# Kernel tuning notes

Hardware: AMD Instinct MI355X
Metric: run time of the kernel (lower is better)

The kernel has to match this reference:

```python
import jax, jax.numpy as jnp
import numpy as np

B, T, D_IN, D_OUT, H = 128, 128, 64, 64, 1024


def _lstm_cell(x_t, h, c, W_ih, W_hh, b_ih, b_hh):
    # PyTorch LSTMCell: gates = x@W_ih^T + b_ih + h@W_hh^T + b_hh, order [i, f, g, o]
    g = x_t @ W_ih.T + b_ih + h @ W_hh.T + b_hh  # [B, 4H]
    i, f, gg, o = jnp.split(g, 4, axis=-1)
    c_new = jax.nn.sigmoid(f) * c + jax.nn.sigmoid(i) * jnp.tanh(gg)
    h_new = jax.nn.sigmoid(o) * jnp.tanh(c_new)
    return h_new, c_new


def setup_inputs() -> dict:
    key = jax.random.key(0)
    ks = jax.random.split(key, 16)
    s_in = 1.0 / np.sqrt(H)
    inp = {
        "x": jax.random.normal(ks[0], (B, T, D_IN), dtype=jnp.float32),
        "W_ih1": jax.random.normal(ks[1], (4 * H, D_IN), dtype=jnp.float32) * s_in,
        "W_hh1": jax.random.normal(ks[2], (4 * H, H), dtype=jnp.float32) * s_in,
        "b_ih1": jax.random.normal(ks[3], (4 * H,), dtype=jnp.float32) * s_in,
        "b_hh1": jax.random.normal(ks[4], (4 * H,), dtype=jnp.float32) * s_in,
        "W_ih2": jax.random.normal(ks[5], (4 * H, H), dtype=jnp.float32) * s_in,
        "W_hh2": jax.random.normal(ks[6], (4 * H, H), dtype=jnp.float32) * s_in,
        "b_ih2": jax.random.normal(ks[7], (4 * H,), dtype=jnp.float32) * s_in,
        "b_hh2": jax.random.normal(ks[8], (4 * H,), dtype=jnp.float32) * s_in,
        "W_lin": jax.random.normal(ks[9], (D_IN, H), dtype=jnp.float32) * s_in,
        "b_lin": jax.random.normal(ks[10], (D_IN,), dtype=jnp.float32) * s_in,
        "W_hio": jax.random.normal(ks[11], (D_OUT, H), dtype=jnp.float32) * s_in,
        "b_hio": jax.random.normal(ks[12], (D_OUT,), dtype=jnp.float32) * s_in,
        "future": 1,
    }
    return inp


def reference(x, W_ih1, W_hh1, b_ih1, b_hh1, W_ih2, W_hh2, b_ih2, b_hh2,
              W_lin, b_lin, W_hio, b_hio, future):
    b = x.shape[0]
    h1 = jnp.zeros((b, H), x.dtype)
    c1 = jnp.zeros((b, H), x.dtype)
    h2 = jnp.zeros((b, H), x.dtype)
    c2 = jnp.zeros((b, H), x.dtype)

    def step(carry, x_t):
        h1, c1, h2, c2 = carry
        h1, c1 = _lstm_cell(x_t, h1, c1, W_ih1, W_hh1, b_ih1, b_hh1)
        h2, c2 = _lstm_cell(h1, h2, c2, W_ih2, W_hh2, b_ih2, b_hh2)
        return (h1, c1, h2, c2), None

    (h1, c1, h2, c2), _ = jax.lax.scan(step, (h1, c1, h2, c2),
                                       jnp.swapaxes(x, 0, 1))  # scan over T
    output = h2 @ W_lin.T + b_lin  # [B, D_IN] (only last step's value is used)

    for _ in range(int(future)):
        h1, c1 = _lstm_cell(output, h1, c1, W_ih1, W_hh1, b_ih1, b_hh1)
        h2, c2 = _lstm_cell(h1, h2, c2, W_ih2, W_hh2, b_ih2, b_hh2)
        output = h2 @ W_hio.T + b_hio  # [B, D_OUT]

    return output[:, None, :]  # [B, 1, D_OUT]
```

## Files before the change

kernel.cpp:

```cpp
#include <hip/hip_runtime.h>

#define B_   128
#define T_   128
#define DIN  64
#define H_   1024
#define NBLK 256
#define NTHR 1024

typedef _Float16 f16;
typedef _Float16 half8 __attribute__((ext_vector_type(8)));
typedef float float4v __attribute__((ext_vector_type(4)));
typedef unsigned uint2v __attribute__((ext_vector_type(2)));
typedef unsigned uint4v __attribute__((ext_vector_type(4)));

#define OFF_W2    34816
#define OFF_SG1A  100352
#define OFF_SG1B  109056
#define OFF_SG2A  117760
#define OFF_SG2B  126464
#define OFF_C1    135168
#define OFF_C2    137216
#define OFF_B1    139264
#define OFF_B2    139328
#define SMEM_BYTES 139392

struct Params {
  const float *x, *Wih1, *Whh1, *bih1, *bhh1, *Wih2, *Whh2, *bih2, *bhh2,
              *Wlin, *blin, *Whio, *bhio;
  const int* fut;
  float* out;
  f16 *x16, *h1a, *h1b, *h2a, *h2b, *ob;
  unsigned *arrive, *rel;
  unsigned *S;
  float* PB;
  unsigned* FL;
};

__device__ __forceinline__ float sigm(float v) { return 1.f / (1.f + __expf(-v)); }
__device__ __forceinline__ float tanh_(float v) { return 2.f / (1.f + __expf(-2.f * v)) - 1.f; }

__device__ __forceinline__ unsigned get_xcc() {
  unsigned x;
  asm volatile("s_getreg_b32 %0, hwreg(HW_REG_XCC_ID)" : "=s"(x));
  return x & 15u;
}

__device__ __forceinline__ void grid_sync(unsigned* arrive, unsigned* rel, unsigned ph) {
  __syncthreads();
  const int tid = threadIdx.x, bid = blockIdx.x;
  if (bid == 0) {
    if (tid > 0 && tid < NBLK) {
      while (__hip_atomic_load(&arrive[tid], __ATOMIC_RELAXED, __HIP_MEMORY_SCOPE_AGENT) != ph)
        __builtin_amdgcn_s_sleep(8);
    }
    __syncthreads();
    if (tid == 0)
      __hip_atomic_store(rel, ph, __ATOMIC_RELEASE, __HIP_MEMORY_SCOPE_AGENT);
  } else {
    if (tid == 0) {
      __hip_atomic_store(&arrive[bid], ph, __ATOMIC_RELEASE, __HIP_MEMORY_SCOPE_AGENT);
      while (__hip_atomic_load(rel, __ATOMIC_RELAXED, __HIP_MEMORY_SCOPE_AGENT) != ph)
        __builtin_amdgcn_s_sleep(8);
    }
  }
  __syncthreads();
  __builtin_amdgcn_fence(__ATOMIC_ACQUIRE, "agent");
}

__device__ __forceinline__ void fast_sync(unsigned* S, unsigned x, unsigned xtotal,
                                          unsigned nxcd, unsigned ph) {
  __syncthreads();
  if (threadIdx.x == 0) {
    unsigned t = __hip_atomic_fetch_add(&S[x * 32], 1u, __ATOMIC_RELAXED, __HIP_MEMORY_SCOPE_AGENT);
    bool leader = (t % xtotal == 0u);
    if ((t + 1u) % xtotal == 0u) {
      unsigned c = __hip_atomic_fetch_add(&S[512], 1u, __ATOMIC_RELAXED, __HIP_MEMORY_SCOPE_AGENT);
      if ((c + 1u) % nxcd == 0u)
        __hip_atomic_store(&S[544], ph, __ATOMIC_RELAXED, __HIP_MEMORY_SCOPE_AGENT);
      asm volatile("buffer_inv sc0 sc1\n\ts_waitcnt vmcnt(0)" ::: "memory");
      __hip_atomic_store(&S[1088 + x * 32], ph, __ATOMIC_RELAXED, __HIP_MEMORY_SCOPE_AGENT);
    }
    if (leader) {
      while (__hip_atomic_load(&S[544], __ATOMIC_RELAXED, __HIP_MEMORY_SCOPE_AGENT) != ph)
        __builtin_amdgcn_s_sleep(1);
      while (__hip_atomic_load(&S[1088 + x * 32], __ATOMIC_RELAXED, __HIP_MEMORY_SCOPE_AGENT) != ph)
        __builtin_amdgcn_s_sleep(1);
      __hip_atomic_store(&S[576 + x * 32], ph, __ATOMIC_RELAXED, __HIP_MEMORY_SCOPE_AGENT);
      asm volatile("buffer_inv sc0\n\ts_waitcnt vmcnt(0)" ::: "memory");
    } else {
      while (__hip_atomic_load(&S[576 + x * 32], __ATOMIC_RELAXED, __HIP_MEMORY_SCOPE_AGENT) != ph)
        __builtin_amdgcn_s_sleep(2);
      asm volatile("buffer_inv sc0\n\ts_waitcnt vmcnt(0)" ::: "memory");
    }
  }
  __syncthreads();
}

__global__ void __launch_bounds__(NTHR, 4) lstm_k(Params p) {
  extern __shared__ char smem[];
  f16*   W1s  = (f16*)(smem);
  f16*   W2s  = (f16*)(smem + OFF_W2);
  float* Sg1A = (float*)(smem + OFF_SG1A);
  float* Sg1B = (float*)(smem + OFF_SG1B);
  float* Sg2A = (float*)(smem + OFF_SG2A);
  float* Sg2B = (float*)(smem + OFF_SG2B);
  float* c1   = (float*)(smem + OFF_C1);
  float* c2   = (float*)(smem + OFF_C2);
  float* bs1  = (float*)(smem + OFF_B1);
  float* bs2  = (float*)(smem + OFF_B2);

  const int tid = threadIdx.x, bid = blockIdx.x;
  const int c   = bid & 127;
  const int g   = bid >> 7;
  const int bidp = bid ^ 128;
  const int cb  = c * 2 + g;
  const int fut = p.fut[0];
  const unsigned xcc = get_xcc();
  unsigned* S = p.S;

  if (bid == 0) {
    for (int i = tid; i < 2048; i += NTHR)
      __hip_atomic_store(&S[i], 0u, __ATOMIC_RELAXED, __HIP_MEMORY_SCOPE_AGENT);
  }
  for (int i = bid * NTHR + tid; i < 256 * 32; i += NBLK * NTHR)
    __hip_atomic_store(&p.FL[i], 0u, __ATOMIC_RELAXED, __HIP_MEMORY_SCOPE_AGENT);

  for (int idx = tid; idx < 17 * 2 * 512; idx += NTHR) {
    int j2 = idx >> 9, r = idx & 511;
    int j = j2 >> 1, nt = j2 & 1;
    int lane_ = r >> 3, jj = r & 7;
    int q = lane_ >> 4, colw = lane_ & 15;
    int row = (colw >> 2) * H_ + c * 8 + nt * 4 + (colw & 3);
    float v = (j < 16) ? p.Whh1[row * H_ + g * 512 + j * 32 + q * 8 + jj]
                       : p.Wih1[row * DIN + g * 32 + q * 8 + jj];
    W1s[idx] = (f16)v;
  }
  for (int idx = tid; idx < 32 * 2 * 512; idx += NTHR) {
    int j2 = idx >> 9, r = idx & 511;
    int j = j2 >> 1, nt = j2 & 1;
    int lane_ = r >> 3, jj = r & 7;
    int q = lane_ >> 4, colw = lane_ & 15;
    int row = (colw >> 2) * H_ + c * 8 + nt * 4 + (colw & 3);
    float v = (j < 16) ? p.Wih2[row * H_ + g * 512 + j * 32 + q * 8 + jj]
                       : p.Whh2[row * H_ + g * 512 + (j - 16) * 32 + q * 8 + jj];
    W2s[idx] = (f16)v;
  }
  if (tid < 16) {
    int row = (tid >> 2) * H_ + c * 8 + g * 4 + (tid & 3);
    bs1[tid] = p.bih1[row] + p.bhh1[row];
    bs2[tid] = p.bih2[row] + p.bhh2[row];
  }
  for (int i = tid; i < 512; i += NTHR) { c1[i] = 0.f; c2[i] = 0.f; }
  for (int i = bid * NTHR + tid; i < B_ * T_ * DIN; i += NBLK * NTHR)
    p.x16[i] = (f16)p.x[i];
  for (int i = bid * NTHR + tid; i < B_ * H_; i += NBLK * NTHR) {
    p.h1a[i] = (f16)0.f; p.h1b[i] = (f16)0.f;
    p.h2a[i] = (f16)0.f; p.h2b[i] = (f16)0.f;
  }

  unsigned ph = 1;
  grid_sync(p.arrive, p.rel, ph);
  if (tid == 0)
    __hip_atomic_fetch_add(&S[1600 + xcc], 1u, __ATOMIC_RELAXED, __HIP_MEMORY_SCOPE_AGENT);
  ++ph;
  grid_sync(p.arrive, p.rel, ph);

  unsigned xtotal = __hip_atomic_load(&S[1600 + xcc], __ATOMIC_RELAXED, __HIP_MEMORY_SCOPE_AGENT);
  unsigned nxcd = 0;
  for (int i = 0; i < 16; ++i)
    nxcd += (__hip_atomic_load(&S[1600 + i], __ATOMIC_RELAXED, __HIP_MEMORY_SCOPE_AGENT) != 0u);

  auto gsync = [&]() { ++ph; fast_sync(S, xcc, xtotal, nxcd, ph); };

  const int lane = tid & 63, wq = tid >> 6;
  const int s  = wq >> 3;
  const int wv = wq & 7;
  const int col = lane & 15, quad = lane >> 4;
  const int m0 = wv * 16 + col;
  const int ko = quad * 8;
  const f16* W1f = W1s + lane * 8;
  const f16* W2f = W2s + lane * 8;
  float* S1w = s ? Sg1B : Sg1A;
  float* S2w = s ? Sg2B : Sg2A;
  const int hoff = quad * 1024 + m0 * 4;

  auto PBidx = [](int cg, int dg, int ss, int ll) {
    return ((((cg * 2 + dg) * 2 + ss) * 2 + ll) * 2048);
  };

  f16 *h1c = p.h1a, *h1n = p.h1b, *h2c = p.h2a, *h2n = p.h2b;
  unsigned pcnt = 0;

  auto lstm_pw = [&](const float* SgA, const float* SgB, float* Pb0, float* Pb1,
                     const float* bsX, float* cst, f16* hn) {
    int idx = tid & 511;
    int mm = idx >> 2, cc = idx & 3;
    int i0 = mm * 17 + cc;
    int pb = mm * 16 + cc;
    float gq[4];
    #pragma unroll
    for (int q = 0; q < 4; ++q) {
      float pv0 = __hip_atomic_load(Pb0 + pb + q * 4, __ATOMIC_RELAXED, __HIP_MEMORY_SCOPE_AGENT);
      float pv1 = __hip_atomic_load(Pb1 + pb + q * 4, __ATOMIC_RELAXED, __HIP_MEMORY_SCOPE_AGENT);
      gq[q] = SgA[i0 + q * 4] + SgB[i0 + q * 4] + pv0 + pv1 + bsX[q * 4 + cc];
    }
    float cn = sigm(gq[1]) * cst[idx] + sigm(gq[0]) * tanh_(gq[2]);
    cst[idx] = cn;
    f16 hv = (f16)(sigm(gq[3]) * tanh_(cn));
    int v = (int)__builtin_bit_cast(unsigned short, hv);
    int base = lane & ~3;
    int v0 = __shfl(v, base, 64),     v1 = __shfl(v, base + 1, 64);
    int v2 = __shfl(v, base + 2, 64), v3 = __shfl(v, base + 3, 64);
    if (cc == 0) {
      unsigned long long pk = (unsigned long long)(unsigned short)v0
        | ((unsigned long long)(unsigned short)v1 << 16)
        | ((unsigned long long)(unsigned short)v2 << 32)
        | ((unsigned long long)(unsigned short)v3 << 48);
      __hip_atomic_store((unsigned long long*)(hn + cb * 512 + mm * 4), pk,
                         __ATOMIC_RELAXED, __HIP_MEMORY_SCOPE_AGENT);
    }
  };

  auto ldwin = [&](const f16* hX, int j) -> half8 {
    const uint2v* q0 = (const uint2v*)(hX + j * 4096 + hoff);
    const uint2v* q1 = (const uint2v*)(hX + j * 4096 + hoff + 512);
    uint2v u0 = *q0, u1 = *q1;
    uint4v u = {u0[0], u0[1], u1[0], u1[1]};
    return __builtin_bit_cast(half8, u);
  };

  auto phase = [&](bool l1, bool l2, const f16* xp, int xstr) {
    ++pcnt;
    float4v a1A = {0,0,0,0}, a1B = {0,0,0,0};
    float4v a2A = {0,0,0,0}, a2B = {0,0,0,0};

    if (l1 && s == 0) {
      half8 ax = *(const half8*)(xp + m0 * xstr + g * 32 + ko);
      a1A = __builtin_amdgcn_mfma_f32_16x16x32_f16(ax, *(const half8*)(W1f + 32 * 512), a1A, 0, 0, 0);
      a1B = __builtin_amdgcn_mfma_f32_16x16x32_f16(ax, *(const half8*)(W1f + 33 * 512), a1B, 0, 0, 0);
    }
    #pragma unroll
    for (int i = 0; i < 8; ++i) {
      int j = s * 8 + i;
      int gw = g * 16 + j;
      half8 w1 = ldwin(h1c, gw);
      if (l1) {
        a1A = __builtin_amdgcn_mfma_f32_16x16x32_f16(w1, *(const half8*)(W1f + (j * 2) * 512), a1A, 0, 0, 0);
        a1B = __builtin_amdgcn_mfma_f32_16x16x32_f16(w1, *(const half8*)(W1f + (j * 2 + 1) * 512), a1B, 0, 0, 0);
      }
      if (l2) {
        half8 w2 = ldwin(h2c, gw);
        a2A = __builtin_amdgcn_mfma_f32_16x16x32_f16(w1, *(const half8*)(W2f + (j * 2) * 512), a2A, 0, 0, 0);
        a2B = __builtin_amdgcn_mfma_f32_16x16x32_f16(w1, *(const half8*)(W2f + (j * 2 + 1) * 512), a2B, 0, 0, 0);
        a2A = __builtin_amdgcn_mfma_f32_16x16x32_f16(w2, *(const half8*)(W2f + ((16 + j) * 2) * 512), a2A, 0, 0, 0);
        a2B = __builtin_amdgcn_mfma_f32_16x16x32_f16(w2, *(const half8*)(W2f + ((16 + j) * 2 + 1) * 512), a2B, 0, 0, 0);
      }
    }

    {
      int mb = (wv * 16 + quad * 4) * 16 + col;
      if (l1) {
        float4v pa = g ? a1A : a1B;
        float* dst = p.PB + PBidx(c, 1 - g, s, 0) + mb;
        #pragma unroll
        for (int r = 0; r < 4; ++r)
          __hip_atomic_store(dst + r * 16, pa[r], __ATOMIC_RELAXED, __HIP_MEMORY_SCOPE_AGENT);
      }
      if (l2) {
        float4v pa = g ? a2A : a2B;
        float* dst = p.PB + PBidx(c, 1 - g, s, 1) + mb;
        #pragma unroll
        for (int r = 0; r < 4; ++r)
          __hip_atomic_store(dst + r * 16, pa[r], __ATOMIC_RELAXED, __HIP_MEMORY_SCOPE_AGENT);
      }
    }
    __syncthreads();
    if (tid == 0)
      __hip_atomic_store(&p.FL[bid * 32], pcnt, __ATOMIC_RELEASE, __HIP_MEMORY_SCOPE_AGENT);

    if (l1) {
      float4v oa = g ? a1B : a1A;
      #pragma unroll
      for (int r = 0; r < 4; ++r)
        S1w[(wv * 16 + quad * 4 + r) * 17 + col] = oa[r];
    }
    if (l2) {
      float4v oa = g ? a2B : a2A;
      #pragma unroll
      for (int r = 0; r < 4; ++r)
        S2w[(wv * 16 + quad * 4 + r) * 17 + col] = oa[r];
    }
    __syncthreads();

    while (__hip_atomic_load(&p.FL[bidp * 32], __ATOMIC_RELAXED, __HIP_MEMORY_SCOPE_AGENT) < pcnt)
      __builtin_amdgcn_s_sleep(1);

    if (tid < 512) {
      if (l1) lstm_pw(Sg1A, Sg1B,
                      p.PB + PBidx(c, g, 0, 0), p.PB + PBidx(c, g, 1, 0),
                      bs1, c1, h1n);
    } else {
      if (l2) lstm_pw(Sg2A, Sg2B,
                      p.PB + PBidx(c, g, 0, 1), p.PB + PBidx(c, g, 1, 1),
                      bs2, c2, h2n);
    }
  };

  auto out_phase = [&](const float* W, const float* bv, bool wout) {
    if (tid >= 512) return;
    int j = bid & 63, mgp = bid >> 6;
    int rid = tid >> 4, ks = tid & 15;
    int mrow = mgp * 32 + rid;
    const float* wr = W + j * H_ + ks * 64;
    float sacc = 0.f;
    #pragma unroll
    for (int q = 0; q < 16; ++q) {
      const uint2v* hp = (const uint2v*)(h2c + (ks * 16 + q) * 512 + mrow * 4);
      uint2v u = *hp;
      half8 hv4;
      { uint4v t = {u[0], u[1], 0u, 0u}; hv4 = __builtin_bit_cast(half8, t); }
      sacc += (float)hv4[0] * wr[q * 4 + 0] + (float)hv4[1] * wr[q * 4 + 1]
            + (float)hv4[2] * wr[q * 4 + 2] + (float)hv4[3] * wr[q * 4 + 3];
    }
    sacc += __shfl_down(sacc, 8, 16);
    sacc += __shfl_down(sacc, 4, 16);
    sacc += __shfl_down(sacc, 2, 16);
    sacc += __shfl_down(sacc, 1, 16);
    if (ks == 0) {
      float v = sacc + bv[j];
      f16 hv = (f16)v;
      __hip_atomic_store((unsigned short*)&p.ob[mrow * 64 + j],
                         __builtin_bit_cast(unsigned short, hv),
                         __ATOMIC_RELAXED, __HIP_MEMORY_SCOPE_AGENT);
      if (wout) p.out[mrow * 64 + j] = v;
    }
  };

  for (int t = -1; t < T_; ++t) {
    bool l1 = (t + 1 < T_), l2 = (t >= 0);
    phase(l1, l2, p.x16 + (t + 1) * DIN, T_ * DIN);
    gsync();
    if (l1) { f16* tm = h1c; h1c = h1n; h1n = tm; }
    if (l2) { f16* tm = h2c; h2c = h2n; h2n = tm; }
  }
  out_phase(p.Wlin, p.blin, fut == 0);
  gsync();
  for (int f = 0; f < fut; ++f) {
    phase(true, false, p.ob, 64);
    gsync();
    { f16* tm = h1c; h1c = h1n; h1n = tm; }
    phase(false, true, p.ob, 64);
    gsync();
    { f16* tm = h2c; h2c = h2n; h2n = tm; }
    out_phase(p.Whio, p.bhio, f == fut - 1);
    gsync();
  }
}

extern "C" void kernel_launch(void* const* d_in, const int* in_sizes, int n_in,
                              void* d_out, int out_size, void* d_ws, size_t ws_size,
                              hipStream_t stream) {
  char* w = (char*)d_ws;
  auto carve = [&](size_t n) { char* r = w; w += (n + 255) & ~(size_t)255; return r; };

  Params p;
  p.x    = (const float*)d_in[0];
  p.Wih1 = (const float*)d_in[1];
  p.Whh1 = (const float*)d_in[2];
  p.bih1 = (const float*)d_in[3];
  p.bhh1 = (const float*)d_in[4];
  p.Wih2 = (const float*)d_in[5];
  p.Whh2 = (const float*)d_in[6];
  p.bih2 = (const float*)d_in[7];
  p.bhh2 = (const float*)d_in[8];
  p.Wlin = (const float*)d_in[9];
  p.blin = (const float*)d_in[10];
  p.Whio = (const float*)d_in[11];
  p.bhio = (const float*)d_in[12];
  p.fut  = (const int*)d_in[13];
  p.out  = (float*)d_out;

  p.x16 = (f16*)carve((size_t)B_ * T_ * DIN * 2);
  p.h1a = (f16*)carve((size_t)B_ * H_ * 2);
  p.h1b = (f16*)carve((size_t)B_ * H_ * 2);
  p.h2a = (f16*)carve((size_t)B_ * H_ * 2);
  p.h2b = (f16*)carve((size_t)B_ * H_ * 2);
  p.ob  = (f16*)carve((size_t)B_ * 64 * 2);
  p.arrive = (unsigned*)carve(NBLK * sizeof(unsigned));
  p.rel    = (unsigned*)carve(256);
  p.S      = (unsigned*)carve(2048 * sizeof(unsigned));
  p.PB     = (float*)carve((size_t)128 * 2 * 2 * 2 * 2048 * sizeof(float));
  p.FL     = (unsigned*)carve((size_t)256 * 32 * sizeof(unsigned));

  (void)hipFuncSetAttribute((const void*)lstm_k,
                            hipFuncAttributeMaxDynamicSharedMemorySize, SMEM_BYTES);
  void* args[] = { &p };
  (void)hipLaunchCooperativeKernel((void*)lstm_k, dim3(NBLK), dim3(NTHR),
                                   args, SMEM_BYTES, stream);
}
```

Before: 1.890 ms.

## Use system-scope atomic accesses for shared data instead of cache invalidates in grid sync

Removes the explicit buffer_inv cache invalidations from the cross-block barrier. In exchange, every cross-block exchange (hidden states, partial gate sums, flags, output buffer) becomes a system-scope relaxed atomic load or store, so it bypasses the non-coherent caches. The aim is to make each per-timestep barrier cheaper. The cost is that each data access now goes further out to memory, and barrier correctness now relies on these accesses being coherent.

Measured after the change: 1.859 ms, median of 2. Within noise of the previous version (-1.6%).

```diff
diff --git a/kernel.cpp b/kernel.cpp
--- a/kernel.cpp
+++ b/kernel.cpp
@@ -12,6 +12,7 @@
 typedef float float4v __attribute__((ext_vector_type(4)));
 typedef unsigned uint2v __attribute__((ext_vector_type(2)));
 typedef unsigned uint4v __attribute__((ext_vector_type(4)));
+typedef unsigned long long u64;
 
 #define OFF_W2    34816
 #define OFF_SG1A  100352
@@ -45,6 +46,13 @@
   return x & 15u;
 }
 
+__device__ __forceinline__ u64 sysld(const void* p_) {
+  return __hip_atomic_load((const u64*)p_, __ATOMIC_RELAXED, __HIP_MEMORY_SCOPE_SYSTEM);
+}
+__device__ __forceinline__ void sysst(void* p_, u64 v) {
+  __hip_atomic_store((u64*)p_, v, __ATOMIC_RELAXED, __HIP_MEMORY_SCOPE_SYSTEM);
+}
+
 __device__ __forceinline__ void grid_sync(unsigned* arrive, unsigned* rel, unsigned ph) {
   __syncthreads();
   const int tid = threadIdx.x, bid = blockIdx.x;
@@ -77,7 +85,6 @@
       unsigned c = __hip_atomic_fetch_add(&S[512], 1u, __ATOMIC_RELAXED, __HIP_MEMORY_SCOPE_AGENT);
       if ((c + 1u) % nxcd == 0u)
         __hip_atomic_store(&S[544], ph, __ATOMIC_RELAXED, __HIP_MEMORY_SCOPE_AGENT);
-      asm volatile("buffer_inv sc0 sc1\n\ts_waitcnt vmcnt(0)" ::: "memory");
       __hip_atomic_store(&S[1088 + x * 32], ph, __ATOMIC_RELAXED, __HIP_MEMORY_SCOPE_AGENT);
     }
     if (leader) {
@@ -86,11 +93,9 @@
       while (__hip_atomic_load(&S[1088 + x * 32], __ATOMIC_RELAXED, __HIP_MEMORY_SCOPE_AGENT) != ph)
         __builtin_amdgcn_s_sleep(1);
       __hip_atomic_store(&S[576 + x * 32], ph, __ATOMIC_RELAXED, __HIP_MEMORY_SCOPE_AGENT);
-      asm volatile("buffer_inv sc0\n\ts_waitcnt vmcnt(0)" ::: "memory");
     } else {
       while (__hip_atomic_load(&S[576 + x * 32], __ATOMIC_RELAXED, __HIP_MEMORY_SCOPE_AGENT) != ph)
         __builtin_amdgcn_s_sleep(2);
-      asm volatile("buffer_inv sc0\n\ts_waitcnt vmcnt(0)" ::: "memory");
     }
   }
   __syncthreads();
@@ -122,8 +127,8 @@
     for (int i = tid; i < 2048; i += NTHR)
       __hip_atomic_store(&S[i], 0u, __ATOMIC_RELAXED, __HIP_MEMORY_SCOPE_AGENT);
   }
-  for (int i = bid * NTHR + tid; i < 256 * 32; i += NBLK * NTHR)
-    __hip_atomic_store(&p.FL[i], 0u, __ATOMIC_RELAXED, __HIP_MEMORY_SCOPE_AGENT);
+  for (int i = bid * NTHR + tid; i < 256 * 32 / 2; i += NBLK * NTHR)
+    sysst(&p.FL[i * 2], 0ull);
 
   for (int idx = tid; idx < 17 * 2 * 512; idx += NTHR) {
     int j2 = idx >> 9, r = idx & 511;
@@ -153,9 +158,9 @@
   for (int i = tid; i < 512; i += NTHR) { c1[i] = 0.f; c2[i] = 0.f; }
   for (int i = bid * NTHR + tid; i < B_ * T_ * DIN; i += NBLK * NTHR)
     p.x16[i] = (f16)p.x[i];
-  for (int i = bid * NTHR + tid; i < B_ * H_; i += NBLK * NTHR) {
-    p.h1a[i] = (f16)0.f; p.h1b[i] = (f16)0.f;
-    p.h2a[i] = (f16)0.f; p.h2b[i] = (f16)0.f;
+  for (int i = bid * NTHR + tid; i < B_ * H_ / 4; i += NBLK * NTHR) {
+    sysst((u64*)p.h1a + i, 0ull); sysst((u64*)p.h1b + i, 0ull);
+    sysst((u64*)p.h2a + i, 0ull); sysst((u64*)p.h2b + i, 0ull);
   }
 
   unsigned ph = 1;
@@ -200,8 +205,8 @@
     float gq[4];
     #pragma unroll
     for (int q = 0; q < 4; ++q) {
-      float pv0 = __hip_atomic_load(Pb0 + pb + q * 4, __ATOMIC_RELAXED, __HIP_MEMORY_SCOPE_AGENT);
-      float pv1 = __hip_atomic_load(Pb1 + pb + q * 4, __ATOMIC_RELAXED, __HIP_MEMORY_SCOPE_AGENT);
+      float pv0 = __hip_atomic_load(Pb0 + pb + q * 4, __ATOMIC_RELAXED, __HIP_MEMORY_SCOPE_SYSTEM);
+      float pv1 = __hip_atomic_load(Pb1 + pb + q * 4, __ATOMIC_RELAXED, __HIP_MEMORY_SCOPE_SYSTEM);
       gq[q] = SgA[i0 + q * 4] + SgB[i0 + q * 4] + pv0 + pv1 + bsX[q * 4 + cc];
     }
     float cn = sigm(gq[1]) * cst[idx] + sigm(gq[0]) * tanh_(gq[2]);
@@ -212,30 +217,40 @@
     int v0 = __shfl(v, base, 64),     v1 = __shfl(v, base + 1, 64);
     int v2 = __shfl(v, base + 2, 64), v3 = __shfl(v, base + 3, 64);
     if (cc == 0) {
-      unsigned long long pk = (unsigned long long)(unsigned short)v0
-        | ((unsigned long long)(unsigned short)v1 << 16)
-        | ((unsigned long long)(unsigned short)v2 << 32)
-        | ((unsigned long long)(unsigned short)v3 << 48);
-      __hip_atomic_store((unsigned long long*)(hn + cb * 512 + mm * 4), pk,
-                         __ATOMIC_RELAXED, __HIP_MEMORY_SCOPE_AGENT);
+      u64 pk = (u64)(unsigned short)v0
+        | ((u64)(unsigned short)v1 << 16)
+        | ((u64)(unsigned short)v2 << 32)
+        | ((u64)(unsigned short)v3 << 48);
+      sysst(hn + cb * 512 + mm * 4, pk);
     }
   };
 
   auto ldwin = [&](const f16* hX, int j) -> half8 {
-    const uint2v* q0 = (const uint2v*)(hX + j * 4096 + hoff);
-    const uint2v* q1 = (const uint2v*)(hX + j * 4096 + hoff + 512);
-    uint2v u0 = *q0, u1 = *q1;
-    uint4v u = {u0[0], u0[1], u1[0], u1[1]};
+    u64 u0 = sysld(hX + j * 4096 + hoff);
+    u64 u1 = sysld(hX + j * 4096 + hoff + 512);
+    uint2v a0 = __builtin_bit_cast(uint2v, u0);
+    uint2v a1 = __builtin_bit_cast(uint2v, u1);
+    uint4v u = {a0[0], a0[1], a1[0], a1[1]};
     return __builtin_bit_cast(half8, u);
   };
 
-  auto phase = [&](bool l1, bool l2, const f16* xp, int xstr) {
+  auto phase = [&](bool l1, bool l2, const f16* xp, int xstr, bool xb) {
     ++pcnt;
     float4v a1A = {0,0,0,0}, a1B = {0,0,0,0};
     float4v a2A = {0,0,0,0}, a2B = {0,0,0,0};
 
     if (l1 && s == 0) {
-      half8 ax = *(const half8*)(xp + m0 * xstr + g * 32 + ko);
+      half8 ax;
+      if (xb) {
+        u64 u0 = sysld(xp + m0 * xstr + g * 32 + ko);
+        u64 u1 = sysld(xp + m0 * xstr + g * 32 + ko + 4);
+        uint2v a0 = __builtin_bit_cast(uint2v, u0);
+        uint2v a1v = __builtin_bit_cast(uint2v, u1);
+        uint4v u = {a0[0], a0[1], a1v[0], a1v[1]};
+        ax = __builtin_bit_cast(half8, u);
+      } else {
+        ax = *(const half8*)(xp + m0 * xstr + g * 32 + ko);
+      }
       a1A = __builtin_amdgcn_mfma_f32_16x16x32_f16(ax, *(const half8*)(W1f + 32 * 512), a1A, 0, 0, 0);
       a1B = __builtin_amdgcn_mfma_f32_16x16x32_f16(ax, *(const half8*)(W1f + 33 * 512), a1B, 0, 0, 0);
     }
@@ -264,19 +279,19 @@
         float* dst = p.PB + PBidx(c, 1 - g, s, 0) + mb;
         #pragma unroll
         for (int r = 0; r < 4; ++r)
-          __hip_atomic_store(dst + r * 16, pa[r], __ATOMIC_RELAXED, __HIP_MEMORY_SCOPE_AGENT);
+          __hip_atomic_store(dst + r * 16, pa[r], __ATOMIC_RELAXED, __HIP_MEMORY_SCOPE_SYSTEM);
       }
       if (l2) {
         float4v pa = g ? a2A : a2B;
         float* dst = p.PB + PBidx(c, 1 - g, s, 1) + mb;
         #pragma unroll
         for (int r = 0; r < 4; ++r)
-          __hip_atomic_store(dst + r * 16, pa[r], __ATOMIC_RELAXED, __HIP_MEMORY_SCOPE_AGENT);
+          __hip_atomic_store(dst + r * 16, pa[r], __ATOMIC_RELAXED, __HIP_MEMORY_SCOPE_SYSTEM);
       }
     }
     __syncthreads();
     if (tid == 0)
-      __hip_atomic_store(&p.FL[bid * 32], pcnt, __ATOMIC_RELEASE, __HIP_MEMORY_SCOPE_AGENT);
+      __hip_atomic_store(&p.FL[bid * 32], pcnt, __ATOMIC_RELEASE, __HIP_MEMORY_SCOPE_SYSTEM);
 
     if (l1) {
       float4v oa = g ? a1B : a1A;
@@ -292,7 +307,7 @@
     }
     __syncthreads();
 
-    while (__hip_atomic_load(&p.FL[bidp * 32], __ATOMIC_RELAXED, __HIP_MEMORY_SCOPE_AGENT) < pcnt)
+    while (__hip_atomic_load(&p.FL[bidp * 32], __ATOMIC_RELAXED, __HIP_MEMORY_SCOPE_SYSTEM) < pcnt)
       __builtin_amdgcn_s_sleep(1);
 
     if (tid < 512) {
@@ -315,10 +330,10 @@
     float sacc = 0.f;
     #pragma unroll
     for (int q = 0; q < 16; ++q) {
-      const uint2v* hp = (const uint2v*)(h2c + (ks * 16 + q) * 512 + mrow * 4);
-      uint2v u = *hp;
+      u64 uv = sysld(h2c + (ks * 16 + q) * 512 + mrow * 4);
+      uint2v uu = __builtin_bit_cast(uint2v, uv);
       half8 hv4;
-      { uint4v t = {u[0], u[1], 0u, 0u}; hv4 = __builtin_bit_cast(half8, t); }
+      { uint4v t = {uu[0], uu[1], 0u, 0u}; hv4 = __builtin_bit_cast(half8, t); }
       sacc += (float)hv4[0] * wr[q * 4 + 0] + (float)hv4[1] * wr[q * 4 + 1]
             + (float)hv4[2] * wr[q * 4 + 2] + (float)hv4[3] * wr[q * 4 + 3];
     }
@@ -329,16 +344,16 @@
     if (ks == 0) {
       float v = sacc + bv[j];
       f16 hv = (f16)v;
-      __hip_atomic_store((unsigned short*)&p.ob[mrow * 64 + j],
-                         __builtin_bit_cast(unsigned short, hv),
-                         __ATOMIC_RELAXED, __HIP_MEMORY_SCOPE_AGENT);
+      unsigned short hb16 = __builtin_bit_cast(unsigned short, hv);
+      __hip_atomic_store((unsigned short*)&p.ob[mrow * 64 + j], hb16,
+                         __ATOMIC_RELAXED, __HIP_MEMORY_SCOPE_SYSTEM);
       if (wout) p.out[mrow * 64 + j] = v;
     }
   };
 
   for (int t = -1; t < T_; ++t) {
     bool l1 = (t + 1 < T_), l2 = (t >= 0);
-    phase(l1, l2, p.x16 + (t + 1) * DIN, T_ * DIN);
+    phase(l1, l2, p.x16 + (t + 1) * DIN, T_ * DIN, false);
     gsync();
     if (l1) { f16* tm = h1c; h1c = h1n; h1n = tm; }
     if (l2) { f16* tm = h2c; h2c = h2n; h2n = tm; }
@@ -346,10 +361,10 @@
   out_phase(p.Wlin, p.blin, fut == 0);
   gsync();
   for (int f = 0; f < fut; ++f) {
-    phase(true, false, p.ob, 64);
+    phase(true, false, p.ob, 64, true);
     gsync();
     { f16* tm = h1c; h1c = h1n; h1n = tm; }
-    phase(false, true, p.ob, 64);
+    phase(false, true, p.ob, 64, true);
     gsync();
     { f16* tm = h2c; h2c = h2n; h2n = tm; }
     out_phase(p.Whio, p.bhio, f == fut - 1);
```
